# Kernel tuning notes

Hardware: AMD Instinct MI355X
Metric: run time of the kernel (lower is better)

The kernel has to match this reference:

```python
import jax, jax.numpy as jnp
import numpy as np
from jax import lax

B, S, D = 4, 4096, 2048
R, E, K, H = 256, 8, 2, 512
MAX_BLEND = 0.9


def setup_inputs() -> dict:
    key = jax.random.key(0)
    ks = jax.random.split(key, 11)
    def w(k, shape, fan_in):
        return jax.random.normal(k, shape, dtype=jnp.float32) * (1.0 / np.sqrt(fan_in))
    return {
        "h": jax.random.normal(ks[0], (B, S, D), dtype=jnp.float32),
        "V": w(ks[1], (D, R), D),            # down-projection (z = V^T h)
        "U": w(ks[2], (R, D), R),            # reconstruction (h = U z)
        "Wr": w(ks[3], (R, E), R),           # router
        "br": jnp.zeros((E,), dtype=jnp.float32),
        "W1": w(ks[4], (E, R, H), R),        # per-expert up-proj
        "b1": jnp.zeros((E, H), dtype=jnp.float32),
        "W2": w(ks[5], (E, H, R), H),        # per-expert down-proj
        "b2": jnp.zeros((E, R), dtype=jnp.float32),
        "Wh": w(ks[6], (D, 1), D),           # halting unit
        "bh": jnp.zeros((1,), dtype=jnp.float32),
    }


def _forward(h, V, U, Wr, br, W1, b1, W2, b2, Wh, bh):
    b, s, d = h.shape
    T = b * s
    # 1. project to vein subspace: z = V^T h  -> [B,S,R]
    z = jnp.einsum("bsd,dr->bsr", h, V)
    zf = z.reshape(T, R)
    # 2. top-k routing
    logits = zf @ Wr + br                      # [T,E]
    probs = jax.nn.softmax(logits, axis=-1)
    topw, topi = lax.top_k(probs, K)           # [T,K]
    topw = topw / jnp.sum(topw, axis=-1, keepdims=True)
    combine = jnp.zeros((T, E), dtype=zf.dtype).at[jnp.arange(T)[:, None], topi].add(topw)
    # 3. expert mix (dense-compute reference; combine is K-sparse per token)
    hidden = jax.nn.gelu(jnp.einsum("tr,erh->teh", zf, W1) + b1, approximate=False)
    expert_out = jnp.einsum("teh,ehr->ter", hidden, W2) + b2    # [T,E,R]
    z_new = jnp.einsum("te,ter->tr", combine, expert_out).reshape(b, s, R)
    # 4. residual blend: blend = min(top_k/num_experts, max_blend)
    blend = min(K / E, MAX_BLEND)
    z_final = z_new * blend + z * (1.0 - blend)
    # 5. reconstruct + halting
    h_new = jnp.einsum("bsr,rd->bsd", z_final, U)
    p_halt = jax.nn.sigmoid(jnp.einsum("bsd,do->bso", h_new, Wh) + bh)
    return h_new, p_halt


def reference(h, V, U, Wr, br, W1, b1, W2, b2, Wh, bh):
    return _forward(h, V, U, Wr, br, W1, b1, W2, b2, Wh, bh)
```

## Files before the change

### kernel.cpp

```cpp
#include <hip/hip_runtime.h>
#include <stdint.h>
#include <math.h>

#define TK 16384
#define DD 2048
#define RR 256
#define EE 8
#define HH 512
#define NSEG_MAX 264
#define NPAIR_MAX (NSEG_MAX * 128)

typedef __attribute__((ext_vector_type(4))) float f32x4;
typedef __attribute__((ext_vector_type(8))) short s16x8;
typedef __attribute__((ext_vector_type(8))) unsigned short u16x8;
typedef __attribute__((ext_vector_type(4))) unsigned u32x4;
typedef unsigned short ushort_t;

__device__ inline unsigned short f2bf(float f) {
  union { float f; unsigned u; } v; v.f = f;
  unsigned r = v.u + 0x7fffu + ((v.u >> 16) & 1u);
  return (unsigned short)(r >> 16);
}
__device__ inline float bf2f(ushort_t u) {
  union { unsigned u; float f; } v; v.u = ((unsigned)u) << 16; return v.f;
}

__device__ inline void gll16(const void* g, void* l) {
  __builtin_amdgcn_global_load_lds(
      (const __attribute__((address_space(1))) void*)g,
      (__attribute__((address_space(3))) void*)l, 16, 0, 0);
}

__device__ inline u16x8 pack8(f32x4 a, f32x4 b) {
  u16x8 r;
  r[0] = f2bf(a.x); r[1] = f2bf(a.y); r[2] = f2bf(a.z); r[3] = f2bf(a.w);
  r[4] = f2bf(b.x); r[5] = f2bf(b.y); r[6] = f2bf(b.z); r[7] = f2bf(b.w);
  return r;
}

#define SWZ8(idx) (((idx & 7) ^ ((idx >> 3) & 7)) * 8)

__global__ __launch_bounds__(256) void k_prep(
    const float* __restrict__ V, const float* __restrict__ U,
    const float* __restrict__ W1, const float* __restrict__ W2,
    const float* __restrict__ Wr, const float* __restrict__ Wh,
    ushort_t* __restrict__ Vt, ushort_t* __restrict__ Ut,
    ushort_t* __restrict__ W1t, ushort_t* __restrict__ W2t,
    float* __restrict__ VeffT, float* __restrict__ Uh,
    u32x4* __restrict__ zbase) {
  __shared__ float sm[2112];
  int b = blockIdx.x, t = threadIdx.x;
  if (b < 3072) {
    const float* src; ushort_t* dst; int nr, nc, c0, r0;
    if (b < 512)       { src = V; dst = Vt; nr = 2048; nc = 256;
                         c0 = (b & 7) * 32; r0 = (b >> 3) * 32; }
    else if (b < 1024) { int bx = b - 512; src = U; dst = Ut; nr = 256; nc = 2048;
                         c0 = (bx & 63) * 32; r0 = (bx >> 6) * 32; }
    else if (b < 2048) { int bx = b - 1024; int s = bx >> 7; bx &= 127;
                         src = W1 + (size_t)s * 131072; dst = W1t + (size_t)s * 131072;
                         nr = 256; nc = 512; c0 = (bx & 15) * 32; r0 = (bx >> 4) * 32; }
    else               { int bx = b - 2048; int s = bx >> 7; bx &= 127;
                         src = W2 + (size_t)s * 131072; dst = W2t + (size_t)s * 131072;
                         nr = 512; nc = 256; c0 = (bx & 7) * 32; r0 = (bx >> 3) * 32; }
    int tx = t & 31, ty = t >> 5;
    #pragma unroll
    for (int i = 0; i < 32; i += 8)
      sm[(ty + i) * 33 + tx] = src[(size_t)(r0 + ty + i) * nc + c0 + tx];
    __syncthreads();
    #pragma unroll
    for (int i = 0; i < 32; i += 8)
      dst[(size_t)(c0 + ty + i) * nr + r0 + tx] = f2bf(sm[tx * 33 + ty + i]);
  } else if (b < 3080) {
    #pragma unroll
    for (int i = 0; i < 8; ++i) sm[i * 256 + t] = Wr[i * 256 + t];
    __syncthreads();
    int d = (b - 3072) * 256 + t;
    float a[8] = {0, 0, 0, 0, 0, 0, 0, 0};
    const float* vrow = V + (size_t)d * RR;
    for (int r = 0; r < RR; r += 4) {
      f32x4 v = *(const f32x4*)(vrow + r);
      #pragma unroll
      for (int e = 0; e < 8; ++e)
        a[e] += v.x * sm[r * 8 + e] + v.y * sm[(r + 1) * 8 + e] +
                v.z * sm[(r + 2) * 8 + e] + v.w * sm[(r + 3) * 8 + e];
    }
    #pragma unroll
    for (int e = 0; e < 8; ++e) VeffT[(size_t)e * DD + d] = a[e];
  } else if (b < 3144) {
    int wave = t >> 6, lane = t & 63;
    int r = (b - 3080) * 4 + wave;
    const f32x4* u4 = (const f32x4*)(U + (size_t)r * DD);
    const f32x4* w4 = (const f32x4*)Wh;
    float acc = 0.f;
    #pragma unroll
    for (int it = 0; it < 8; ++it) {
      f32x4 a = u4[it * 64 + lane], bb = w4[it * 64 + lane];
      acc += a.x * bb.x + a.y * bb.y + a.z * bb.z + a.w * bb.w;
    }
    #pragma unroll
    for (int o = 32; o; o >>= 1) acc += __shfl_down(acc, o, 64);
    if (lane == 0) Uh[r] = acc;
  } else {
    int i = (b - 3144) * 256 + t;
    zbase[i] = (u32x4){0u, 0u, 0u, 0u};
  }
}

__global__ __launch_bounds__(256, 2) void k_front(
    const float* __restrict__ h, const ushort_t* __restrict__ Vt,
    const float* __restrict__ VeffT, const float* __restrict__ br,
    ushort_t* __restrict__ zb, int* __restrict__ topi, float* __restrict__ topw,
    int* __restrict__ ctrl) {
  __shared__ ushort_t As[2][32 * 72];
  __shared__ ushort_t Bs[2][256 * 64];
  __shared__ float Vs[2][512];
  __shared__ int lcnt[8];
  int t = threadIdx.x;
  int m0 = blockIdx.x * 32;
  int lane = t & 63, wave = t >> 6;
  int ln = lane & 15, hi = lane >> 4;
  const int xo = (ln & 7) << 3;
  int arow = t >> 3, koff = (t & 7) * 8;
  const float* aptr = h + (size_t)(m0 + arow) * DD + koff;
  if (t < 8) lcnt[t] = 0;

  f32x4 acc[2][4];
  #pragma unroll
  for (int i = 0; i < 2; ++i)
    #pragma unroll
    for (int j = 0; j < 4; ++j) acc[i][j] = (f32x4){0.f, 0.f, 0.f, 0.f};
  float racc[8] = {0, 0, 0, 0, 0, 0, 0, 0};

  f32x4 pc0, pc1, pn0, pn1;
  {
    pc0 = ((const f32x4*)aptr)[0];
    pc1 = ((const f32x4*)aptr)[1];
    #pragma unroll
    for (int u = 0; u < 8; ++u) {
      int idx = u * 256 + t;
      gll16(Vt + (size_t)(idx >> 3) * DD + SWZ8(idx), &Bs[0][idx * 8]);
    }
    if (t < 128) gll16(VeffT + (size_t)(t >> 4) * DD + (t & 15) * 4, &Vs[0][t * 4]);
    *(u16x8*)&As[0][arow * 72 + koff] = pack8(pc0, pc1);
  }
  __syncthreads();

  for (int s = 0; s < 32; ++s) {
    int cb = s & 1, xb = cb ^ 1;
    int k1 = (s + 1) * 64;
    if (s < 31) {
      pn0 = ((const f32x4*)(aptr + k1))[0];
      pn1 = ((const f32x4*)(aptr + k1))[1];
      #pragma unroll
      for (int u = 0; u < 8; ++u) {
        int idx = u * 256 + t;
        gll16(Vt + (size_t)(idx >> 3) * DD + k1 + SWZ8(idx), &Bs[xb][idx * 8]);
      }
      if (t < 128) gll16(VeffT + (size_t)(t >> 4) * DD + k1 + (t & 15) * 4, &Vs[xb][t * 4]);
    }
    {
      const f32x4* vsb = (const f32x4*)&Vs[cb][0];
      #pragma unroll
      for (int e = 0; e < 8; ++e) {
        f32x4 v0 = vsb[(e * 64 + koff) >> 2];
        f32x4 v1 = vsb[((e * 64 + koff) >> 2) + 1];
        racc[e] += pc0.x * v0.x + pc0.y * v0.y + pc0.z * v0.z + pc0.w * v0.w +
                   pc1.x * v1.x + pc1.y * v1.y + pc1.z * v1.z + pc1.w * v1.w;
      }
    }
    #pragma unroll
    for (int ks = 0; ks < 2; ++ks) {
      s16x8 af[2], bq[4];
      #pragma unroll
      for (int i = 0; i < 2; ++i)
        af[i] = *(const s16x8*)&As[cb][(i * 16 + ln) * 72 + ks * 32 + hi * 8];
      #pragma unroll
      for (int j = 0; j < 4; ++j)
        bq[j] = *(const s16x8*)&Bs[cb][(wave * 64 + j * 16 + ln) * 64 + ((ks * 32 + hi * 8) ^ xo)];
      #pragma unroll
      for (int i = 0; i < 2; ++i)
        #pragma unroll
        for (int j = 0; j < 4; ++j)
          acc[i][j] = __builtin_amdgcn_mfma_f32_16x16x32_bf16(af[i], bq[j], acc[i][j], 0, 0, 0);
    }
    if (s < 31) {
      *(u16x8*)&As[xb][arow * 72 + koff] = pack8(pn0, pn1);
      pc0 = pn0; pc1 = pn1;
    }
    __syncthreads();
  }

  #pragma unroll
  for (int i = 0; i < 2; ++i)
    #pragma unroll
    for (int j = 0; j < 4; ++j)
      #pragma unroll
      for (int r = 0; r < 4; ++r) {
        int row = m0 + i * 16 + hi * 4 + r;
        int col = wave * 64 + j * 16 + ln;
        zb[(size_t)row * RR + col] = f2bf(acc[i][j][r]);
      }

  #pragma unroll
  for (int e = 0; e < 8; ++e) {
    racc[e] += __shfl_xor(racc[e], 1, 64);
    racc[e] += __shfl_xor(racc[e], 2, 64);
    racc[e] += __shfl_xor(racc[e], 4, 64);
  }
  if ((t & 7) == 0) {
    int token = m0 + arow;
    f32x4 br0 = ((const f32x4*)br)[0], br1 = ((const f32x4*)br)[1];
    float l[8] = {racc[0] + br0.x, racc[1] + br0.y, racc[2] + br0.z, racc[3] + br0.w,
                  racc[4] + br1.x, racc[5] + br1.y, racc[6] + br1.z, racc[7] + br1.w};
    float best = -1e30f; int bi = 0;
    #pragma unroll
    for (int e = 0; e < 8; ++e) if (l[e] > best) { best = l[e]; bi = e; }
    float sec = -1e30f; int si = 0;
    #pragma unroll
    for (int e = 0; e < 8; ++e) if (e != bi && l[e] > sec) { sec = l[e]; si = e; }
    float w0 = 1.f / (1.f + expf(sec - best));
    topi[token * 2 + 0] = bi; topi[token * 2 + 1] = si;
    topw[token * 2 + 0] = w0; topw[token * 2 + 1] = 1.f - w0;
    atomicAdd(&lcnt[bi], 1);
    atomicAdd(&lcnt[si], 1);
  }
  __syncthreads();
  if (t < 8) atomicAdd(&ctrl[t], lcnt[t]);
}

__global__ __launch_bounds__(256) void k_bases(int* ctrl) {
  __shared__ int sb[8], se[8];
  int t = threadIdx.x;
  if (t < 8) {
    int segs = (ctrl[t] + 127) >> 7;
    int scan = segs;
    #pragma unroll
    for (int o = 1; o < 8; o <<= 1) {
      int u2 = __shfl_up(scan, o, 64);
      if (t >= o) scan += u2;
    }
    int start = scan - segs;
    ctrl[8 + t] = start << 7;
    sb[t] = start; se[t] = scan;
  }
  __syncthreads();
  for (int sg = t; sg < NSEG_MAX; sg += 256) {
    int e = -1;
    #pragma unroll
    for (int k = 0; k < 8; ++k)
      if (sg >= sb[k] && sg < se[k]) e = k;
    ctrl[16 + sg] = e;
  }
}

__global__ __launch_bounds__(256) void k_scatter(const int* topi, const float* topw,
                                                 int* ctrl, int* pair_t, float* pair_w,
                                                 int* inv) {
  __shared__ int lcnt[8], lbase[8];
  int t = threadIdx.x;
  if (t < 8) lcnt[t] = 0;
  __syncthreads();
  int slot = blockIdx.x * 256 + t;
  int e = topi[slot];
  float wv = topw[slot];
  int lp = atomicAdd(&lcnt[e], 1);
  __syncthreads();
  if (t < 8) lbase[t] = atomicAdd(&ctrl[8 + t], lcnt[t]);
  __syncthreads();
  int p = lbase[e] + lp;
  pair_t[p] = slot >> 1;
  pair_w[p] = wv;
  inv[slot] = p;
}

#define GEMM_COMPUTE(AS, BS)                                                          \
  _Pragma("unroll")                                                                   \
  for (int ks = 0; ks < 2; ++ks) {                                                    \
    s16x8 af[4], bq[4];                                                               \
    _Pragma("unroll")                                                                 \
    for (int i = 0; i < 4; ++i)                                                       \
      af[i] = *(const s16x8*)&AS[(wr * 64 + i * 16 + ln) * 64 + ((ks * 32 + hi * 8) ^ xo)]; \
    _Pragma("unroll")                                                                 \
    for (int j = 0; j < 4; ++j)                                                       \
      bq[j] = *(const s16x8*)&BS[(wc * 64 + j * 16 + ln) * 64 + ((ks * 32 + hi * 8) ^ xo)]; \
    _Pragma("unroll")                                                                 \
    for (int i = 0; i < 4; ++i)                                                       \
      _Pragma("unroll")                                                               \
      for (int j = 0; j < 4; ++j)                                                     \
        acc[i][j] = __builtin_amdgcn_mfma_f32_16x16x32_bf16(af[i], bq[j], acc[i][j], 0, 0, 0); \
  }

__global__ __launch_bounds__(256, 2) void k_e1(const ushort_t* zb, const ushort_t* W1t,
                                               const float* b1, const int* ctrl,
                                               const int* pair_t, ushort_t* hidden) {
  __shared__ ushort_t As[2][8192];
  __shared__ ushort_t Bs[2][8192];
  __shared__ int pt[128];
  int sg = blockIdx.x >> 2, nt = blockIdx.x & 3;
  int e = ctrl[16 + sg];
  if (e < 0) return;
  int t = threadIdx.x;
  if (t < 128) pt[t] = pair_t[sg * 128 + t];
  __syncthreads();
  int n0 = nt * 128;
  const ushort_t* Bbase = W1t + (size_t)e * HH * RR;
  int lane = t & 63, wave = t >> 6;
  int wr = wave >> 1, wc = wave & 1;
  int ln = lane & 15, hi = lane >> 4;
  const int xo = (ln & 7) << 3;

  f32x4 acc[4][4];
  #pragma unroll
  for (int i = 0; i < 4; ++i)
    #pragma unroll
    for (int j = 0; j < 4; ++j) acc[i][j] = (f32x4){0.f, 0.f, 0.f, 0.f};

  #pragma unroll
  for (int u = 0; u < 4; ++u) {
    int idx = u * 256 + t;
    gll16(zb + (size_t)pt[idx >> 3] * RR + SWZ8(idx), &As[0][idx * 8]);
    gll16(Bbase + (size_t)(n0 + (idx >> 3)) * RR + SWZ8(idx), &Bs[0][idx * 8]);
  }
  __syncthreads();
  for (int s = 0; s < 4; ++s) {
    int cb = s & 1, xb = cb ^ 1;
    if (s < 3) {
      int k1 = (s + 1) * 64;
      #pragma unroll
      for (int u = 0; u < 4; ++u) {
        int idx = u * 256 + t;
        gll16(zb + (size_t)pt[idx >> 3] * RR + k1 + SWZ8(idx), &As[xb][idx * 8]);
        gll16(Bbase + (size_t)(n0 + (idx >> 3)) * RR + k1 + SWZ8(idx), &Bs[xb][idx * 8]);
      }
    }
    GEMM_COMPUTE(As[cb], Bs[cb]);
    __syncthreads();
  }
  #pragma unroll
  for (int i = 0; i < 4; ++i)
    #pragma unroll
    for (int j = 0; j < 4; ++j)
      #pragma unroll
      for (int r = 0; r < 4; ++r) {
        int pl = wr * 64 + i * 16 + hi * 4 + r;
        int col = n0 + wc * 64 + j * 16 + ln;
        float v = acc[i][j][r] + b1[e * HH + col];
        float g = 0.5f * v * (1.f + erff(v * 0.70710678118654752f));
        hidden[(size_t)(sg * 128 + pl) * HH + col] = f2bf(g);
      }
}

__global__ __launch_bounds__(256, 2) void k_e2(const ushort_t* hidden, const ushort_t* W2t,
                                               const float* b2, const int* ctrl,
                                               const int* pair_t, const float* pair_w,
                                               ushort_t* eout) {
  __shared__ ushort_t As[2][8192];
  __shared__ ushort_t Bs[2][8192];
  __shared__ float pw[128];
  int sg = blockIdx.x >> 1, nt = blockIdx.x & 1;
  int e = ctrl[16 + sg];
  if (e < 0) return;
  int t = threadIdx.x;
  if (t < 128) pw[t] = pair_w[sg * 128 + t];
  __syncthreads();
  int n0 = nt * 128;
  const ushort_t* Abase = hidden + (size_t)sg * 128 * HH;
  const ushort_t* Bbase = W2t + (size_t)e * RR * HH;
  int lane = t & 63, wave = t >> 6;
  int wr = wave >> 1, wc = wave & 1;
  int ln = lane & 15, hi = lane >> 4;
  const int xo = (ln & 7) << 3;

  f32x4 acc[4][4];
  #pragma unroll
  for (int i = 0; i < 4; ++i)
    #pragma unroll
    for (int j = 0; j < 4; ++j) acc[i][j] = (f32x4){0.f, 0.f, 0.f, 0.f};

  #pragma unroll
  for (int u = 0; u < 4; ++u) {
    int idx = u * 256 + t;
    gll16(Abase + (size_t)(idx >> 3) * HH + SWZ8(idx), &As[0][idx * 8]);
    gll16(Bbase + (size_t)(n0 + (idx >> 3)) * HH + SWZ8(idx), &Bs[0][idx * 8]);
  }
  __syncthreads();
  for (int s = 0; s < 8; ++s) {
    int cb = s & 1, xb = cb ^ 1;
    if (s < 7) {
      int k1 = (s + 1) * 64;
      #pragma unroll
      for (int u = 0; u < 4; ++u) {
        int idx = u * 256 + t;
        gll16(Abase + (size_t)(idx >> 3) * HH + k1 + SWZ8(idx), &As[xb][idx * 8]);
        gll16(Bbase + (size_t)(n0 + (idx >> 3)) * HH + k1 + SWZ8(idx), &Bs[xb][idx * 8]);
      }
    }
    GEMM_COMPUTE(As[cb], Bs[cb]);
    __syncthreads();
  }
  #pragma unroll
  for (int i = 0; i < 4; ++i)
    #pragma unroll
    for (int j = 0; j < 4; ++j)
      #pragma unroll
      for (int r = 0; r < 4; ++r) {
        int pl = wr * 64 + i * 16 + hi * 4 + r;
        int col = n0 + wc * 64 + j * 16 + ln;
        float v = acc[i][j][r] + b2[e * RR + col];
        eout[(size_t)(sg * 128 + pl) * RR + col] = f2bf(pw[pl] * v);
      }
}

__global__ __launch_bounds__(256) void k_final(const ushort_t* __restrict__ zb,
                                               const ushort_t* __restrict__ eout,
                                               const int* __restrict__ inv,
                                               const float* __restrict__ Uh,
                                               const float* __restrict__ bh,
                                               ushort_t* __restrict__ zb2,
                                               float* __restrict__ phalt) {
  __shared__ float luh[256];
  int t = threadIdx.x;
  if (t < 64) ((f32x4*)luh)[t] = ((const f32x4*)Uh)[t];
  __syncthreads();
  int tok = blockIdx.x * 64 + (t >> 2), q = t & 3;
  int i0 = inv[tok * 2], i1 = inv[tok * 2 + 1];
  const u16x8* z8 = (const u16x8*)(zb + (size_t)tok * RR + q * 64);
  const u16x8* ea = (const u16x8*)(eout + (size_t)i0 * RR + q * 64);
  const u16x8* eb = (const u16x8*)(eout + (size_t)i1 * RR + q * 64);
  ushort_t* o = zb2 + (size_t)tok * RR + q * 64;
  float acc = 0.f;
  #pragma unroll
  for (int it = 0; it < 8; ++it) {
    u16x8 zv = z8[it], av = ea[it], bv = eb[it];
    u16x8 pk;
    #pragma unroll
    for (int j = 0; j < 8; ++j) {
      float zf = 0.75f * bf2f(zv[j]) + 0.25f * (bf2f(av[j]) + bf2f(bv[j]));
      acc += zf * luh[q * 64 + it * 8 + j];
      pk[j] = f2bf(zf);
    }
    *(u16x8*)(o + it * 8) = pk;
  }
  acc += __shfl_xor(acc, 1, 64);
  acc += __shfl_xor(acc, 2, 64);
  if (q == 0) phalt[tok] = 1.f / (1.f + expf(-(acc + bh[0])));
}

__global__ __launch_bounds__(256, 2) void k_gemm_u(const ushort_t* zb2, const ushort_t* Ut,
                                                   float* outp) {
  __shared__ ushort_t As[2][8192];
  __shared__ ushort_t Bs[2][8192];
  int hw = blockIdx.x;
  int bid = (hw & 7) * 256 + (hw >> 3);
  int mt = bid >> 4, nt = bid & 15;
  int m0 = mt * 128, n0 = nt * 128;
  int t = threadIdx.x;
  int lane = t & 63, wave = t >> 6;
  int wr = wave >> 1, wc = wave & 1;
  int ln = lane & 15, hi = lane >> 4;
  const int xo = (ln & 7) << 3;

  f32x4 acc[4][4];
  #pragma unroll
  for (int i = 0; i < 4; ++i)
    #pragma unroll
    for (int j = 0; j < 4; ++j) acc[i][j] = (f32x4){0.f, 0.f, 0.f, 0.f};

  #pragma unroll
  for (int u = 0; u < 4; ++u) {
    int idx = u * 256 + t;
    gll16(zb2 + (size_t)(m0 + (idx >> 3)) * RR + SWZ8(idx), &As[0][idx * 8]);
    gll16(Ut + (size_t)(n0 + (idx >> 3)) * RR + SWZ8(idx), &Bs[0][idx * 8]);
  }
  __syncthreads();
  for (int s = 0; s < 4; ++s) {
    int cb = s & 1, xb = cb ^ 1;
    if (s < 3) {
      int k1 = (s + 1) * 64;
      #pragma unroll
      for (int u = 0; u < 4; ++u) {
        int idx = u * 256 + t;
        gll16(zb2 + (size_t)(m0 + (idx >> 3)) * RR + k1 + SWZ8(idx), &As[xb][idx * 8]);
        gll16(Ut + (size_t)(n0 + (idx >> 3)) * RR + k1 + SWZ8(idx), &Bs[xb][idx * 8]);
      }
    }
    GEMM_COMPUTE(As[cb], Bs[cb]);
    __syncthreads();
  }
  #pragma unroll
  for (int i = 0; i < 4; ++i)
    #pragma unroll
    for (int j = 0; j < 4; ++j)
      #pragma unroll
      for (int r = 0; r < 4; ++r) {
        int row = m0 + wr * 64 + i * 16 + hi * 4 + r;
        int col = n0 + wc * 64 + j * 16 + ln;
        outp[(size_t)row * DD + col] = acc[i][j][r];
      }
}

extern "C" void kernel_launch(void* const* d_in, const int* in_sizes, int n_in,
                              void* d_out, int out_size, void* d_ws, size_t ws_size,
                              hipStream_t stream) {
  (void)in_sizes; (void)n_in; (void)out_size;
  const float* h  = (const float*)d_in[0];
  const float* V  = (const float*)d_in[1];
  const float* U  = (const float*)d_in[2];
  const float* Wr = (const float*)d_in[3];
  const float* br = (const float*)d_in[4];
  const float* W1 = (const float*)d_in[5];
  const float* b1 = (const float*)d_in[6];
  const float* W2 = (const float*)d_in[7];
  const float* b2 = (const float*)d_in[8];
  const float* Wh = (const float*)d_in[9];
  const float* bh = (const float*)d_in[10];
  float* outp = (float*)d_out;
  char* w = (char*)d_ws;

  constexpr size_t OFF_VT    = 0;
  constexpr size_t OFF_UT    = 1048576;
  constexpr size_t OFF_W1T   = 2097152;
  constexpr size_t OFF_W2T   = 4194304;
  constexpr size_t OFF_VEFFT = 6291456;
  constexpr size_t OFF_UHV   = 6356992;
  constexpr size_t OFF_TOPI  = 6361088;
  constexpr size_t OFF_TOPW  = 6492160;
  constexpr size_t OFF_INV   = 6623232;
  constexpr size_t OFF_CTRL  = 6754304;
  constexpr size_t OFF_PT    = 6758400;
  constexpr size_t OFF_PW    = 6893568;
  constexpr size_t OFF_ZB    = 7028736;
  constexpr size_t OFF_EOUT  = 15417344;
  constexpr size_t OFF_HID   = 32718848;
  constexpr size_t OFF_ZB2   = OFF_HID;
  constexpr size_t WS_NEED   = 67321856;
  if (ws_size < WS_NEED) return;

  ushort_t* Vt    = (ushort_t*)(w + OFF_VT);
  ushort_t* Ut    = (ushort_t*)(w + OFF_UT);
  ushort_t* W1t   = (ushort_t*)(w + OFF_W1T);
  ushort_t* W2t   = (ushort_t*)(w + OFF_W2T);
  float*    VeffT = (float*)(w + OFF_VEFFT);
  float*    Uh    = (float*)(w + OFF_UHV);
  int*      topi  = (int*)(w + OFF_TOPI);
  float*    topw  = (float*)(w + OFF_TOPW);
  int*      inv   = (int*)(w + OFF_INV);
  int*      ctrl  = (int*)(w + OFF_CTRL);
  int*      pair_t= (int*)(w + OFF_PT);
  float*    pair_w= (float*)(w + OFF_PW);
  ushort_t* zb    = (ushort_t*)(w + OFF_ZB);
  ushort_t* eout  = (ushort_t*)(w + OFF_EOUT);
  ushort_t* hidden= (ushort_t*)(w + OFF_HID);
  ushort_t* zb2   = (ushort_t*)(w + OFF_ZB2);

  k_prep<<<3211, 256, 0, stream>>>(V, U, W1, W2, Wr, Wh, Vt, Ut, W1t, W2t,
                                   VeffT, Uh, (u32x4*)(w + OFF_CTRL));
  k_front<<<512, 256, 0, stream>>>(h, Vt, VeffT, br, zb, topi, topw, ctrl);
  k_bases<<<1, 256, 0, stream>>>(ctrl);
  k_scatter<<<128, 256, 0, stream>>>(topi, topw, ctrl, pair_t, pair_w, inv);
  k_e1<<<NSEG_MAX * 4, 256, 0, stream>>>(zb, W1t, b1, ctrl, pair_t, hidden);
  k_e2<<<NSEG_MAX * 2, 256, 0, stream>>>(hidden, W2t, b2, ctrl, pair_t, pair_w, eout);
  k_final<<<256, 256, 0, stream>>>(zb, eout, inv, Uh, bh, zb2, outp + (size_t)TK * DD);
  k_gemm_u<<<2048, 256, 0, stream>>>(zb2, Ut, outp);
}
```

Measured before the change: 208.7 us.

## Fuse residual blend and halting into the U reconstruction GEMM A-tile load

Removes the separate k_final kernel and builds the blended z tile (0.75*z + 0.25*(expert_a + expert_b)) on the fly inside k_gemm_u. Register-staged global loads feed a padded LDS A tile, and the halting dot product is computed only by nt==0 blocks. This drops one launch and the zb2 write/read round trip. In exchange, each of the 16 column tiles recomputes the blend with three gathered row loads instead of one async copy, and the A-tile loads are no longer asynchronous global-to-LDS.

```diff
diff --git a/kernel.cpp b/kernel.cpp
--- a/kernel.cpp
+++ b/kernel.cpp
@@ -411,45 +411,14 @@
       }
 }
 
-__global__ __launch_bounds__(256) void k_final(const ushort_t* __restrict__ zb,
-                                               const ushort_t* __restrict__ eout,
-                                               const int* __restrict__ inv,
-                                               const float* __restrict__ Uh,
-                                               const float* __restrict__ bh,
-                                               ushort_t* __restrict__ zb2,
-                                               float* __restrict__ phalt) {
+__global__ __launch_bounds__(256, 2) void k_gemm_u(
+    const ushort_t* __restrict__ zb, const ushort_t* __restrict__ eout,
+    const int* __restrict__ inv, const ushort_t* __restrict__ Ut,
+    const float* __restrict__ Uh, const float* __restrict__ bh,
+    float* __restrict__ outp, float* __restrict__ phalt) {
+  __shared__ ushort_t As[2][128 * 72];
+  __shared__ ushort_t Bs[2][8192];
   __shared__ float luh[256];
-  int t = threadIdx.x;
-  if (t < 64) ((f32x4*)luh)[t] = ((const f32x4*)Uh)[t];
-  __syncthreads();
-  int tok = blockIdx.x * 64 + (t >> 2), q = t & 3;
-  int i0 = inv[tok * 2], i1 = inv[tok * 2 + 1];
-  const u16x8* z8 = (const u16x8*)(zb + (size_t)tok * RR + q * 64);
-  const u16x8* ea = (const u16x8*)(eout + (size_t)i0 * RR + q * 64);
-  const u16x8* eb = (const u16x8*)(eout + (size_t)i1 * RR + q * 64);
-  ushort_t* o = zb2 + (size_t)tok * RR + q * 64;
-  float acc = 0.f;
-  #pragma unroll
-  for (int it = 0; it < 8; ++it) {
-    u16x8 zv = z8[it], av = ea[it], bv = eb[it];
-    u16x8 pk;
-    #pragma unroll
-    for (int j = 0; j < 8; ++j) {
-      float zf = 0.75f * bf2f(zv[j]) + 0.25f * (bf2f(av[j]) + bf2f(bv[j]));
-      acc += zf * luh[q * 64 + it * 8 + j];
-      pk[j] = f2bf(zf);
-    }
-    *(u16x8*)(o + it * 8) = pk;
-  }
-  acc += __shfl_xor(acc, 1, 64);
-  acc += __shfl_xor(acc, 2, 64);
-  if (q == 0) phalt[tok] = 1.f / (1.f + expf(-(acc + bh[0])));
-}
-
-__global__ __launch_bounds__(256, 2) void k_gemm_u(const ushort_t* zb2, const ushort_t* Ut,
-                                                   float* outp) {
-  __shared__ ushort_t As[2][8192];
-  __shared__ ushort_t Bs[2][8192];
   int hw = blockIdx.x;
   int bid = (hw & 7) * 256 + (hw >> 3);
   int mt = bid >> 4, nt = bid & 15;
@@ -459,6 +428,14 @@
   int wr = wave >> 1, wc = wave & 1;
   int ln = lane & 15, hi = lane >> 4;
   const int xo = (ln & 7) << 3;
+  int arow = t >> 1, ahalf = t & 1;
+  int tok = m0 + arow;
+  int i0 = inv[tok * 2], i1 = inv[tok * 2 + 1];
+  const ushort_t* zrow = zb + (size_t)tok * RR + ahalf * 32;
+  const ushort_t* earow = eout + (size_t)i0 * RR + ahalf * 32;
+  const ushort_t* ebrow = eout + (size_t)i1 * RR + ahalf * 32;
+  if (t < 64) ((f32x4*)luh)[t] = ((const f32x4*)Uh)[t];
+  float phacc = 0.f;
 
   f32x4 acc[4][4];
   #pragma unroll
@@ -466,27 +443,81 @@
     #pragma unroll
     for (int j = 0; j < 4; ++j) acc[i][j] = (f32x4){0.f, 0.f, 0.f, 0.f};
 
-  #pragma unroll
-  for (int u = 0; u < 4; ++u) {
-    int idx = u * 256 + t;
-    gll16(zb2 + (size_t)(m0 + (idx >> 3)) * RR + SWZ8(idx), &As[0][idx * 8]);
-    gll16(Ut + (size_t)(n0 + (idx >> 3)) * RR + SWZ8(idx), &Bs[0][idx * 8]);
-  }
-  __syncthreads();
+  u16x8 zv[4], av[4], bv[4];
+  {
+    const u16x8* z8 = (const u16x8*)zrow;
+    const u16x8* a8 = (const u16x8*)earow;
+    const u16x8* b8 = (const u16x8*)ebrow;
+    #pragma unroll
+    for (int q = 0; q < 4; ++q) { zv[q] = z8[q]; av[q] = a8[q]; bv[q] = b8[q]; }
+    #pragma unroll
+    for (int u = 0; u < 4; ++u) {
+      int idx = u * 256 + t;
+      gll16(Ut + (size_t)(n0 + (idx >> 3)) * RR + SWZ8(idx), &Bs[0][idx * 8]);
+    }
+    __syncthreads();
+    int kl = ahalf * 32;
+    #pragma unroll
+    for (int q = 0; q < 4; ++q) {
+      u16x8 pk;
+      #pragma unroll
+      for (int j = 0; j < 8; ++j) {
+        float zf = 0.75f * bf2f(zv[q][j]) + 0.25f * (bf2f(av[q][j]) + bf2f(bv[q][j]));
+        if (nt == 0) phacc += zf * luh[kl + q * 8 + j];
+        pk[j] = f2bf(zf);
+      }
+      *(u16x8*)&As[0][arow * 72 + ahalf * 32 + q * 8] = pk;
+    }
+  }
+  __syncthreads();
+
   for (int s = 0; s < 4; ++s) {
     int cb = s & 1, xb = cb ^ 1;
     if (s < 3) {
       int k1 = (s + 1) * 64;
+      const u16x8* z8 = (const u16x8*)(zrow + k1);
+      const u16x8* a8 = (const u16x8*)(earow + k1);
+      const u16x8* b8 = (const u16x8*)(ebrow + k1);
+      #pragma unroll
+      for (int q = 0; q < 4; ++q) { zv[q] = z8[q]; av[q] = a8[q]; bv[q] = b8[q]; }
       #pragma unroll
       for (int u = 0; u < 4; ++u) {
         int idx = u * 256 + t;
-        gll16(zb2 + (size_t)(m0 + (idx >> 3)) * RR + k1 + SWZ8(idx), &As[xb][idx * 8]);
         gll16(Ut + (size_t)(n0 + (idx >> 3)) * RR + k1 + SWZ8(idx), &Bs[xb][idx * 8]);
       }
     }
-    GEMM_COMPUTE(As[cb], Bs[cb]);
+    #pragma unroll
+    for (int ks = 0; ks < 2; ++ks) {
+      s16x8 af[4], bq[4];
+      #pragma unroll
+      for (int i = 0; i < 4; ++i)
+        af[i] = *(const s16x8*)&As[cb][(wr * 64 + i * 16 + ln) * 72 + ks * 32 + hi * 8];
+      #pragma unroll
+      for (int j = 0; j < 4; ++j)
+        bq[j] = *(const s16x8*)&Bs[cb][(wc * 64 + j * 16 + ln) * 64 + ((ks * 32 + hi * 8) ^ xo)];
+      #pragma unroll
+      for (int i = 0; i < 4; ++i)
+        #pragma unroll
+        for (int j = 0; j < 4; ++j)
+          acc[i][j] = __builtin_amdgcn_mfma_f32_16x16x32_bf16(af[i], bq[j], acc[i][j], 0, 0, 0);
+    }
+    if (s < 3) {
+      int kl = (s + 1) * 64 + ahalf * 32;
+      #pragma unroll
+      for (int q = 0; q < 4; ++q) {
+        u16x8 pk;
+        #pragma unroll
+        for (int j = 0; j < 8; ++j) {
+          float zf = 0.75f * bf2f(zv[q][j]) + 0.25f * (bf2f(av[q][j]) + bf2f(bv[q][j]));
+          if (nt == 0) phacc += zf * luh[kl + q * 8 + j];
+          pk[j] = f2bf(zf);
+        }
+        *(u16x8*)&As[xb][arow * 72 + ahalf * 32 + q * 8] = pk;
+      }
+    }
     __syncthreads();
   }
+
   #pragma unroll
   for (int i = 0; i < 4; ++i)
     #pragma unroll
@@ -497,6 +528,12 @@
         int col = n0 + wc * 64 + j * 16 + ln;
         outp[(size_t)row * DD + col] = acc[i][j][r];
       }
+
+  if (nt == 0) {
+    phacc += __shfl_xor(phacc, 1, 64);
+    if (ahalf == 0)
+      phalt[tok] = 1.f / (1.f + expf(-(phacc + bh[0])));
+  }
 }
 
 extern "C" void kernel_launch(void* const* d_in, const int* in_sizes, int n_in,
@@ -532,7 +569,6 @@
   constexpr size_t OFF_ZB    = 7028736;
   constexpr size_t OFF_EOUT  = 15417344;
   constexpr size_t OFF_HID   = 32718848;
-  constexpr size_t OFF_ZB2   = OFF_HID;
   constexpr size_t WS_NEED   = 67321856;
   if (ws_size < WS_NEED) return;
 
@@ -551,7 +587,6 @@
   ushort_t* zb    = (ushort_t*)(w + OFF_ZB);
   ushort_t* eout  = (ushort_t*)(w + OFF_EOUT);
   ushort_t* hidden= (ushort_t*)(w + OFF_HID);
-  ushort_t* zb2   = (ushort_t*)(w + OFF_ZB2);
 
   k_prep<<<3211, 256, 0, stream>>>(V, U, W1, W2, Wr, Wh, Vt, Ut, W1t, W2t,
                                    VeffT, Uh, (u32x4*)(w + OFF_CTRL));
@@ -560,6 +595,6 @@
   k_scatter<<<128, 256, 0, stream>>>(topi, topw, ctrl, pair_t, pair_w, inv);
   k_e1<<<NSEG_MAX * 4, 256, 0, stream>>>(zb, W1t, b1, ctrl, pair_t, hidden);
   k_e2<<<NSEG_MAX * 2, 256, 0, stream>>>(hidden, W2t, b2, ctrl, pair_t, pair_w, eout);
-  k_final<<<256, 256, 0, stream>>>(zb, eout, inv, Uh, bh, zb2, outp + (size_t)TK * DD);
-  k_gemm_u<<<2048, 256, 0, stream>>>(zb2, Ut, outp);
-}
+  k_gemm_u<<<2048, 256, 0, stream>>>(zb, eout, inv, Ut, Uh, bh,
+                                     outp, outp + (size_t)TK * DD);
+}
```

Result: slower. 221.8 us (+6.3%).
